# Optimization experiments

Measured on AMD Instinct MI355X. Metric: run time of the kernel, lower is better.

The kernel has to match this reference:

```python
import jax, jax.numpy as jnp
import numpy as np

K_CORR = 2048        # num_correspondences (init kwarg)
MAX_CORR = 8192      # static pad size for the variable-length nonzero output
THRES_START = 0.5
THRES_STEP = 0.01


def setup_inputs() -> dict:
    key = jax.random.key(0)
    k1, k2, k3 = jax.random.split(key, 3)
    N = M = 8193  # 8192 superpoints + 1 dustbin
    # shift so exp(scores) is mostly well below the 0.5 starting threshold,
    # making the iterative threshold search actually iterate (as in practice
    # with log-domain OT scores)
    matching_scores = jax.random.normal(k1, (N, M), dtype=jnp.float32) - 5.0
    ref_n2p_scores_c = jax.random.uniform(k2, (N - 1,), dtype=jnp.float32)
    src_n2p_scores_c = jax.random.uniform(k3, (M - 1,), dtype=jnp.float32)
    return {
        "matching_scores": matching_scores,
        "ref_n2p_scores_c": ref_n2p_scores_c,
        "src_n2p_scores_c": src_n2p_scores_c,
    }


def _find_thres(inner, k):
    """Replicates: while count(score[:-1,:-1] > thres) < k: thres -= 0.01."""
    def cond(t):
        return jnp.sum(inner > t) < k
    def body(t):
        return t - jnp.float32(THRES_STEP)
    return jax.lax.while_loop(cond, body, jnp.float32(THRES_START))


def reference(matching_scores, ref_n2p_scores_c, src_n2p_scores_c):
    s = jnp.exp(matching_scores)
    # n2p reweighting of the non-dustbin block, as in the torch in-place update
    inner = s[:-1, :-1] * (ref_n2p_scores_c[:, None] * src_n2p_scores_c[None, :])
    # threshold search is discrete -> not differentiated
    thres = _find_thres(jax.lax.stop_gradient(inner), K_CORR)
    mask = inner > thres
    count = jnp.sum(mask)
    # torch returns variable-length nonzero in row-major order; we pad to MAX_CORR
    r, c = jnp.nonzero(mask, size=MAX_CORR, fill_value=0)
    valid = jnp.arange(MAX_CORR) < count
    corr_scores = jnp.where(valid, inner[r, c], 0.0)
    ref_corr_indices = jnp.where(valid, r, -1)
    src_corr_indices = jnp.where(valid, c, -1)
    return ref_corr_indices, src_corr_indices, corr_scores
```

## Files before the change

### kernel.cpp

```cpp
#include <hip/hip_runtime.h>

#define NROWS 8192
#define NCOLS 8192
#define LDIM  8193
#define NBINS 64
#define KCORR 2048
#define MAXC  8192
#define CAP   192
#define FCUT_LOG (-2.5257286443082556f)

#define NQUAD   16781312
#define TILEQ   1024
#define NTILES  16388
#define NGROUPS 262208

__device__ __forceinline__ float inner_val(float m, float rr, float sc) {
    float p = rr * sc;
    return expf(m) * p;
}

__device__ __forceinline__ void fold_thresholds(float* t) {
    float tv = 0.5f;
    for (int n = 0; n < NBINS; ++n) { t[n] = tv; tv = tv - 0.01f; }
}

__device__ __forceinline__ int exact_bin(float v, const float* t) {
    int g = (int)floorf((0.5f - v) * 100.0f) + 1;
    g = (g < 0) ? 0 : ((g > NBINS) ? NBINS : g);
    while (g < NBINS && t[g] >= v) ++g;
    while (g > 0 && t[g - 1] < v) --g;
    return (g > 63) ? 63 : g;
}

__global__ void init_kernel(float* __restrict__ out, unsigned* __restrict__ hist,
                            unsigned* __restrict__ hist2,
                            unsigned* __restrict__ candcnt,
                            unsigned* __restrict__ fullmode) {
    int i = blockIdx.x * blockDim.x + threadIdx.x;
    if (i < 2 * MAXC)       out[i] = -1.0f;
    else if (i < 3 * MAXC)  out[i] = 0.0f;
    if (i < NBINS) { hist[i] = 0u; hist2[i] = 0u; }
    if (i == NBINS) *fullmode = 0u;
    if (i < NROWS) candcnt[i] = 0u;
}

__global__ __launch_bounds__(256) void scan_mask_kernel(
    const float* __restrict__ ms, unsigned long long* __restrict__ masks)
{
    const int tid = threadIdx.x;
    const int lane = tid & 63, wv = tid >> 6;
    const float4* m4 = (const float4*)ms;
    const int g = gridDim.x;

    float4 b0[4], b1[4];
    auto issue = [&](int t, float4* B) {
        const float4* p = m4 + (size_t)t * TILEQ + tid;
        #pragma unroll
        for (int k = 0; k < 4; ++k) B[k] = p[k * 256];
    };
    auto emit = [&](int t, const float4* B) {
        unsigned long long mk0 = __ballot((B[0].x > FCUT_LOG) | (B[0].y > FCUT_LOG) |
                                          (B[0].z > FCUT_LOG) | (B[0].w > FCUT_LOG));
        unsigned long long mk1 = __ballot((B[1].x > FCUT_LOG) | (B[1].y > FCUT_LOG) |
                                          (B[1].z > FCUT_LOG) | (B[1].w > FCUT_LOG));
        unsigned long long mk2 = __ballot((B[2].x > FCUT_LOG) | (B[2].y > FCUT_LOG) |
                                          (B[2].z > FCUT_LOG) | (B[2].w > FCUT_LOG));
        unsigned long long mk3 = __ballot((B[3].x > FCUT_LOG) | (B[3].y > FCUT_LOG) |
                                          (B[3].z > FCUT_LOG) | (B[3].w > FCUT_LOG));
        unsigned long long val = (lane & 2) ? ((lane & 1) ? mk3 : mk2)
                                            : ((lane & 1) ? mk1 : mk0);
        if (lane < 4)
            masks[(size_t)t * 16 + wv * 4 + lane] = val;
    };

    int t = blockIdx.x;
    issue(t, b0);
    while (true) {
        int t1 = t + g;
        if (t1 < NTILES) issue(t1, b1);
        emit(t, b0);
        t = t1;
        if (t >= NTILES) break;
        int t2 = t + g;
        if (t2 < NTILES) issue(t2, b0);
        emit(t, b1);
        t = t2;
        if (t >= NTILES) break;
    }
}

__global__ __launch_bounds__(256) void expand_kernel(
    const float* __restrict__ ms, const float* __restrict__ refs,
    const float* __restrict__ srcs, const unsigned long long* __restrict__ masks,
    unsigned* __restrict__ hist, unsigned* __restrict__ candcnt,
    unsigned* __restrict__ cand_col, float* __restrict__ cand_v, int use_cand)
{
    __shared__ float t[NBINS];
    __shared__ unsigned sub[NBINS];
    int tid = threadIdx.x;
    if (tid == 0) fold_thresholds(t);
    if (tid < NBINS) sub[tid] = 0u;
    __syncthreads();

    for (int i = blockIdx.x * 256 + tid; i < NGROUPS; i += gridDim.x * 256) {
        unsigned long long mask = masks[i];
        if (!mask) continue;
        int tile = i >> 4, r = i & 15, w = r >> 2, k = r & 3;
        int quadBase = tile * TILEQ + k * 256 + w * 64;
        while (mask) {
            int b = __ffsll((long long)mask) - 1;
            mask &= mask - 1;
            int q = quadBase + b;
            float4 v4 = ((const float4*)ms)[q];
            int e0 = q * 4;
            #pragma unroll
            for (int j = 0; j < 4; ++j) {
                float m = (j == 0) ? v4.x : (j == 1) ? v4.y : (j == 2) ? v4.z : v4.w;
                if (!(m > FCUT_LOG)) continue;
                unsigned e = (unsigned)(e0 + j);
                unsigned row = e / 8193u;
                unsigned col = e - row * 8193u;
                if (row >= NROWS || col >= NCOLS) continue;
                float v = inner_val(m, refs[row], srcs[col]);
                atomicAdd(&sub[exact_bin(v, t)], 1u);
                if (use_cand) {
                    unsigned slot = atomicAdd(&candcnt[row], 1u);
                    if (slot < CAP) {
                        cand_col[(size_t)row * CAP + slot] = col;
                        cand_v[(size_t)row * CAP + slot]   = v;
                    }
                }
            }
        }
    }
    __syncthreads();
    if (tid < NBINS && sub[tid]) atomicAdd(&hist[tid], sub[tid]);
}

__global__ void mid_kernel(const unsigned* __restrict__ hist,
                           float* __restrict__ thres, unsigned* __restrict__ nstar,
                           unsigned* __restrict__ fullmode) {
    int tid = threadIdx.x;
    unsigned cum = hist[tid];
    #pragma unroll
    for (int off = 1; off < 64; off <<= 1) {
        unsigned u = __shfl_up(cum, off);
        if (tid >= off) cum += u;
    }
    unsigned long long mk = __ballot(cum >= (unsigned)KCORR);
    if (tid == 0) {
        int nsel = mk ? (int)(__ffsll((long long)mk) - 1) : NBINS;
        if (nsel <= 41) {
            float tv = 0.5f;
            for (int n = 0; n < nsel; ++n) tv = tv - 0.01f;
            *thres = tv; *nstar = (unsigned)nsel; *fullmode = 0u;
        } else {
            *fullmode = 1u; *nstar = 63u; *thres = -1e30f;
        }
    }
}

__global__ __launch_bounds__(256) void fb_hist_kernel(
    const float* __restrict__ ms, const float* __restrict__ refs,
    const float* __restrict__ srcs, const unsigned* __restrict__ fullmode,
    unsigned* __restrict__ hist2)
{
    if (*fullmode == 0u) return;
    __shared__ float t[NBINS];
    __shared__ unsigned sub[64 * 65];
    int tid = threadIdx.x, lane = tid & 63;
    if (tid == 0) fold_thresholds(t);
    for (int i = tid; i < 64 * 65; i += 256) sub[i] = 0u;
    __syncthreads();
    unsigned* mysub = sub + lane * 65;
    for (int q = blockIdx.x * 256 + tid; q < NQUAD; q += gridDim.x * 256) {
        float4 v4 = ((const float4*)ms)[q];
        int e0 = q * 4;
        #pragma unroll
        for (int j = 0; j < 4; ++j) {
            float m = (j == 0) ? v4.x : (j == 1) ? v4.y : (j == 2) ? v4.z : v4.w;
            unsigned e = (unsigned)(e0 + j);
            unsigned row = e / 8193u;
            unsigned col = e - row * 8193u;
            if (row >= NROWS || col >= NCOLS) continue;
            float v = inner_val(m, refs[row], srcs[col]);
            atomicAdd(&mysub[exact_bin(v, t)], 1u);
        }
    }
    __syncthreads();
    if (tid < 64) {
        unsigned s = 0;
        for (int c = 0; c < 64; ++c) s += sub[c * 65 + tid];
        if (s) atomicAdd(&hist2[tid], s);
    }
}

__global__ void mid2_kernel(const unsigned* __restrict__ hist2,
                            const unsigned* __restrict__ fullmode,
                            float* __restrict__ thres, unsigned* __restrict__ nstar) {
    if (*fullmode == 0u) return;
    int tid = threadIdx.x;
    unsigned cum = hist2[tid];
    #pragma unroll
    for (int off = 1; off < 64; off <<= 1) {
        unsigned u = __shfl_up(cum, off);
        if (tid >= off) cum += u;
    }
    unsigned long long mk = __ballot(cum >= (unsigned)KCORR);
    if (tid == 0) {
        int nsel = mk ? (int)(__ffsll((long long)mk) - 1) : (NBINS - 1);
        float tv = 0.5f;
        for (int n = 0; n < nsel; ++n) tv = tv - 0.01f;
        *thres = tv; *nstar = (unsigned)nsel;
    }
}

__global__ __launch_bounds__(256) void rowcnt_kernel(
    const float* __restrict__ ms, const float* __restrict__ refs,
    const float* __restrict__ srcs, const float* __restrict__ thresp,
    const unsigned* __restrict__ fullmode, const unsigned* __restrict__ candcnt,
    const float* __restrict__ cand_v, unsigned* __restrict__ rowcnt, int use_cand)
{
    if (!use_cand || *fullmode != 0u) return;
    int tid = threadIdx.x, wv = tid >> 6, lane = tid & 63;
    int row = blockIdx.x * 4 + wv;
    float th = *thresp;
    unsigned C = candcnt[row];
    unsigned c = 0;
    if (C <= CAP) {
        const float* cv = cand_v + (size_t)row * CAP;
        for (unsigned i = lane; i < C; i += 64) c += (cv[i] > th) ? 1u : 0u;
    } else {
        float rr = refs[row];
        const float* mrow = ms + (size_t)row * LDIM;
        for (int col = lane; col < NCOLS; col += 64)
            c += (inner_val(mrow[col], rr, srcs[col]) > th) ? 1u : 0u;
    }
    #pragma unroll
    for (int off = 32; off > 0; off >>= 1) c += __shfl_down(c, off);
    if (lane == 0) rowcnt[row] = c;
}

__global__ __launch_bounds__(256) void count2_kernel(
    const float* __restrict__ ms, const float* __restrict__ refs,
    const float* __restrict__ srcs, const float* __restrict__ thresp,
    const unsigned* __restrict__ fullmode, unsigned* __restrict__ rowcnt,
    int use_cand)
{
    if (use_cand && *fullmode == 0u) return;
    __shared__ unsigned tot;
    float th = *thresp;
    for (int r4 = 0; r4 < 4; ++r4) {
        int row = blockIdx.x * 4 + r4;
        if (threadIdx.x == 0) tot = 0;
        __syncthreads();
        float rr = refs[row];
        const float* mrow = ms + (size_t)row * LDIM;
        unsigned c = 0;
        for (int col = threadIdx.x; col < NCOLS; col += 256)
            c += (inner_val(mrow[col], rr, srcs[col]) > th) ? 1u : 0u;
        atomicAdd(&tot, c);
        __syncthreads();
        if (threadIdx.x == 0) rowcnt[row] = tot;
        __syncthreads();
    }
}

__global__ __launch_bounds__(1024) void scan_kernel(
    const unsigned* __restrict__ rowcnt, unsigned* __restrict__ rowoff)
{
    __shared__ unsigned ssum[1024];
    int tid = threadIdx.x;
    int r0 = tid * 8;
    unsigned c[8], s = 0;
    #pragma unroll
    for (int k = 0; k < 8; ++k) { c[k] = rowcnt[r0 + k]; s += c[k]; }
    ssum[tid] = s;
    __syncthreads();
    for (int off = 1; off < 1024; off <<= 1) {
        unsigned v = (tid >= off) ? ssum[tid - off] : 0u;
        __syncthreads();
        ssum[tid] += v;
        __syncthreads();
    }
    unsigned excl = ssum[tid] - s;
    #pragma unroll
    for (int k = 0; k < 8; ++k) { rowoff[r0 + k] = excl; excl += c[k]; }
    if (tid == 1023) rowoff[NROWS] = excl;
}

__global__ __launch_bounds__(256) void cwrite_kernel(
    const float* __restrict__ ms, const float* __restrict__ refs,
    const float* __restrict__ srcs, const float* __restrict__ thresp,
    const unsigned* __restrict__ fullmode, const unsigned* __restrict__ rowoff,
    const unsigned* __restrict__ candcnt, const unsigned* __restrict__ cand_col,
    const float* __restrict__ cand_v, float* __restrict__ out, int use_cand)
{
    __shared__ unsigned s_col[4][64];
    __shared__ float    s_val[4][64];
    int tid = threadIdx.x, wv = tid >> 6, lane = tid & 63;
    int row = blockIdx.x * 4 + wv;
    unsigned base = rowoff[row], next = rowoff[row + 1];
    if (base == next || base >= MAXC) return;
    float th = *thresp;
    unsigned k = next - base;
    bool full = (!use_cand) || (*fullmode != 0u) || (candcnt[row] > CAP) || (k > 64);

    if (!full) {
        unsigned C = candcnt[row];
        const unsigned* cc = cand_col + (size_t)row * CAP;
        const float*    cv = cand_v  + (size_t)row * CAP;
        unsigned nrun = 0;
        for (unsigned c0 = 0; c0 < C; c0 += 64) {
            unsigned i = c0 + lane;
            bool sel = false; unsigned col = 0; float v = 0.f;
            if (i < C) { col = cc[i]; v = cv[i]; sel = (v > th); }
            unsigned long long mk = __ballot(sel);
            if (sel) {
                unsigned idx = nrun + (unsigned)__popcll(mk & ((1ull << lane) - 1ull));
                if (idx < 64) { s_col[wv][idx] = col; s_val[wv][idx] = v; }
            }
            nrun += (unsigned)__popcll(mk);
        }
        __builtin_amdgcn_s_waitcnt(0);
        __builtin_amdgcn_wave_barrier();
        unsigned kk = (nrun < k) ? nrun : k;
        if (kk > 64) kk = 64;
        if (lane < (int)kk) {
            unsigned mycol = s_col[wv][lane];
            float    myval = s_val[wv][lane];
            unsigned rank = 0;
            for (unsigned j = 0; j < kk; ++j)
                rank += (s_col[wv][j] < mycol) ? 1u : 0u;
            unsigned pos = base + rank;
            if (pos < MAXC) {
                out[pos]            = (float)row;
                out[MAXC + pos]     = (float)mycol;
                out[2 * MAXC + pos] = myval;
            }
        }
        return;
    }

    float rr = refs[row];
    const float* mrow = ms + (size_t)row * LDIM;
    unsigned running = base;
    for (int c0 = 0; c0 < NCOLS && running < next && running < MAXC; c0 += 64) {
        int col = c0 + lane;
        float v = inner_val(mrow[col], rr, srcs[col]);
        bool pred = v > th;
        unsigned long long mk = __ballot(pred);
        if (pred) {
            unsigned pos = running + (unsigned)__popcll(mk & ((1ull << lane) - 1ull));
            if (pos < MAXC) {
                out[pos]            = (float)row;
                out[MAXC + pos]     = (float)col;
                out[2 * MAXC + pos] = v;
            }
        }
        running += (unsigned)__popcll(mk);
    }
}

extern "C" void kernel_launch(void* const* d_in, const int* in_sizes, int n_in,
                              void* d_out, int out_size, void* d_ws, size_t ws_size,
                              hipStream_t stream) {
    const float* ms  = (const float*)d_in[0];
    const float* ref = (const float*)d_in[1];
    const float* src = (const float*)d_in[2];
    float* out = (float*)d_out;

    char* w = (char*)d_ws;
    unsigned* hist     = (unsigned*)(w);
    unsigned* hist2    = (unsigned*)(w + 256);
    float*    thres    = (float*)(w + 512);
    unsigned* nstar    = (unsigned*)(w + 516);
    unsigned* fullmode = (unsigned*)(w + 520);
    unsigned* rowcnt   = (unsigned*)(w + 1024);
    unsigned* rowoff   = (unsigned*)(w + 1024 + NROWS * 4);
    size_t cc_off = (1024 + (size_t)NROWS * 4 + (size_t)(NROWS + 1) * 4 + 255) & ~(size_t)255;
    unsigned* candcnt = (unsigned*)(w + cc_off);
    size_t mk_off  = cc_off + (size_t)NROWS * 4;
    unsigned long long* masks = (unsigned long long*)(w + mk_off);
    size_t col_off = mk_off + (size_t)NGROUPS * 8;
    unsigned* cand_col = (unsigned*)(w + col_off);
    size_t cv_off  = col_off + (size_t)NROWS * CAP * 4;
    float* cand_v  = (float*)(w + cv_off);
    size_t end_off = cv_off + (size_t)NROWS * CAP * 4;

    int use_mask = (ws_size >= col_off) ? 1 : 0;
    int use_cand = (ws_size >= end_off) ? 1 : 0;

    init_kernel<<<96, 256, 0, stream>>>(out, hist, hist2, candcnt, fullmode);
    if (use_mask) {
        scan_mask_kernel<<<2048, 256, 0, stream>>>(ms, masks);
        expand_kernel<<<1024, 256, 0, stream>>>(ms, ref, src, masks, hist,
                                                candcnt, cand_col, cand_v, use_cand);
    }
    mid_kernel<<<1, 64, 0, stream>>>(hist, thres, nstar, fullmode);
    fb_hist_kernel<<<2048, 256, 0, stream>>>(ms, ref, src, fullmode, hist2);
    mid2_kernel<<<1, 64, 0, stream>>>(hist2, fullmode, thres, nstar);
    rowcnt_kernel<<<NROWS / 4, 256, 0, stream>>>(ms, ref, src, thres, fullmode,
                                                 candcnt, cand_v, rowcnt, use_cand);
    count2_kernel<<<NROWS / 4, 256, 0, stream>>>(ms, ref, src, thres, fullmode,
                                                 rowcnt, use_cand);
    scan_kernel<<<1, 1024, 0, stream>>>(rowcnt, rowoff);
    cwrite_kernel<<<NROWS / 4, 256, 0, stream>>>(ms, ref, src, thres, fullmode,
                                                 rowoff, candcnt, cand_col,
                                                 cand_v, out, use_cand);
}
```

Measured before the change: 431.0 us.

## Fuse mask scan and candidate expansion into one LDS-pipelined streaming kernel

Replaces the two-pass scan_mask + expand kernels with a single dscan kernel. Each wave streams its strided slice of the score matrix into an 8-deep LDS ring via global_load_lds with manual vmcnt waits, and collects above-cutoff elements into a per-block shared buffer. That buffer is then processed for the histogram and per-row candidates. This removes the mask buffer round trip and the second gather read of the matrix. A per-block capacity overflow flag forces the existing full fallback path, which adds a correctness dependency on the candidate density staying under the capacity.

```diff
diff --git a/kernel.cpp b/kernel.cpp
--- a/kernel.cpp
+++ b/kernel.cpp
@@ -7,12 +7,12 @@
 #define KCORR 2048
 #define MAXC  8192
 #define CAP   192
+#define BCAP  448
 #define FCUT_LOG (-2.5257286443082556f)
 
 #define NQUAD   16781312
-#define TILEQ   1024
-#define NTILES  16388
-#define NGROUPS 262208
+#define TOTW    8192
+#define QSTRIDE 524288
 
 __device__ __forceinline__ float inner_val(float m, float rr, float sc) {
     float p = rr * sc;
@@ -32,112 +32,105 @@
     return (g > 63) ? 63 : g;
 }
 
+__device__ __forceinline__ void gl2lds16(const void* g, void* l) {
+    __builtin_amdgcn_global_load_lds(
+        (const __attribute__((address_space(1))) void*)g,
+        (__attribute__((address_space(3))) void*)l, 16, 0, 0);
+}
+
 __global__ void init_kernel(float* __restrict__ out, unsigned* __restrict__ hist,
                             unsigned* __restrict__ hist2,
                             unsigned* __restrict__ candcnt,
-                            unsigned* __restrict__ fullmode) {
+                            unsigned* __restrict__ fullmode,
+                            unsigned* __restrict__ ovfl) {
     int i = blockIdx.x * blockDim.x + threadIdx.x;
     if (i < 2 * MAXC)       out[i] = -1.0f;
     else if (i < 3 * MAXC)  out[i] = 0.0f;
     if (i < NBINS) { hist[i] = 0u; hist2[i] = 0u; }
-    if (i == NBINS) *fullmode = 0u;
+    if (i == NBINS) { *fullmode = 0u; *ovfl = 0u; }
     if (i < NROWS) candcnt[i] = 0u;
 }
 
-__global__ __launch_bounds__(256) void scan_mask_kernel(
-    const float* __restrict__ ms, unsigned long long* __restrict__ masks)
-{
-    const int tid = threadIdx.x;
-    const int lane = tid & 63, wv = tid >> 6;
-    const float4* m4 = (const float4*)ms;
-    const int g = gridDim.x;
-
-    float4 b0[4], b1[4];
-    auto issue = [&](int t, float4* B) {
-        const float4* p = m4 + (size_t)t * TILEQ + tid;
-        #pragma unroll
-        for (int k = 0; k < 4; ++k) B[k] = p[k * 256];
-    };
-    auto emit = [&](int t, const float4* B) {
-        unsigned long long mk0 = __ballot((B[0].x > FCUT_LOG) | (B[0].y > FCUT_LOG) |
-                                          (B[0].z > FCUT_LOG) | (B[0].w > FCUT_LOG));
-        unsigned long long mk1 = __ballot((B[1].x > FCUT_LOG) | (B[1].y > FCUT_LOG) |
-                                          (B[1].z > FCUT_LOG) | (B[1].w > FCUT_LOG));
-        unsigned long long mk2 = __ballot((B[2].x > FCUT_LOG) | (B[2].y > FCUT_LOG) |
-                                          (B[2].z > FCUT_LOG) | (B[2].w > FCUT_LOG));
-        unsigned long long mk3 = __ballot((B[3].x > FCUT_LOG) | (B[3].y > FCUT_LOG) |
-                                          (B[3].z > FCUT_LOG) | (B[3].w > FCUT_LOG));
-        unsigned long long val = (lane & 2) ? ((lane & 1) ? mk3 : mk2)
-                                            : ((lane & 1) ? mk1 : mk0);
-        if (lane < 4)
-            masks[(size_t)t * 16 + wv * 4 + lane] = val;
-    };
-
-    int t = blockIdx.x;
-    issue(t, b0);
-    while (true) {
-        int t1 = t + g;
-        if (t1 < NTILES) issue(t1, b1);
-        emit(t, b0);
-        t = t1;
-        if (t >= NTILES) break;
-        int t2 = t + g;
-        if (t2 < NTILES) issue(t2, b0);
-        emit(t, b1);
-        t = t2;
-        if (t >= NTILES) break;
-    }
-}
-
-__global__ __launch_bounds__(256) void expand_kernel(
-    const float* __restrict__ ms, const float* __restrict__ refs,
-    const float* __restrict__ srcs, const unsigned long long* __restrict__ masks,
-    unsigned* __restrict__ hist, unsigned* __restrict__ candcnt,
-    unsigned* __restrict__ cand_col, float* __restrict__ cand_v, int use_cand)
-{
+__global__ __launch_bounds__(256) void dscan_kernel(
+    const float* __restrict__ ms, const float* __restrict__ refs,
+    const float* __restrict__ srcs, unsigned* __restrict__ hist,
+    unsigned* __restrict__ candcnt, unsigned* __restrict__ cand_col,
+    float* __restrict__ cand_v, unsigned* __restrict__ ovfl, int use_cand)
+{
+    __shared__ float ring[4 * 8 * 256];
     __shared__ float t[NBINS];
     __shared__ unsigned sub[NBINS];
-    int tid = threadIdx.x;
-    if (tid == 0) fold_thresholds(t);
+    __shared__ unsigned s_cnt;
+    __shared__ uint2 pairs[BCAP];
+
+    int tid = threadIdx.x, wv = tid >> 6, lane = tid & 63;
+    if (tid == 0) { fold_thresholds(t); s_cnt = 0u; }
     if (tid < NBINS) sub[tid] = 0u;
     __syncthreads();
 
-    for (int i = blockIdx.x * 256 + tid; i < NGROUPS; i += gridDim.x * 256) {
-        unsigned long long mask = masks[i];
-        if (!mask) continue;
-        int tile = i >> 4, r = i & 15, w = r >> 2, k = r & 3;
-        int quadBase = tile * TILEQ + k * 256 + w * 64;
-        while (mask) {
-            int b = __ffsll((long long)mask) - 1;
-            mask &= mask - 1;
-            int q = quadBase + b;
-            float4 v4 = ((const float4*)ms)[q];
-            int e0 = q * 4;
-            #pragma unroll
-            for (int j = 0; j < 4; ++j) {
-                float m = (j == 0) ? v4.x : (j == 1) ? v4.y : (j == 2) ? v4.z : v4.w;
-                if (!(m > FCUT_LOG)) continue;
-                unsigned e = (unsigned)(e0 + j);
-                unsigned row = e / 8193u;
-                unsigned col = e - row * 8193u;
-                if (row >= NROWS || col >= NCOLS) continue;
-                float v = inner_val(m, refs[row], srcs[col]);
-                atomicAdd(&sub[exact_bin(v, t)], 1u);
-                if (use_cand) {
-                    unsigned slot = atomicAdd(&candcnt[row], 1u);
-                    if (slot < CAP) {
-                        cand_col[(size_t)row * CAP + slot] = col;
-                        cand_v[(size_t)row * CAP + slot]   = v;
-                    }
+    int W = blockIdx.x * 4 + wv;
+    const float4* m4 = (const float4*)ms;
+    float* myring = &ring[wv * (8 * 256)];
+    int nsteps = 32 + ((W < 64) ? 1 : 0);
+
+    auto pushp = [&](unsigned e, float m) {
+        unsigned slot = atomicAdd(&s_cnt, 1u);
+        if (slot < BCAP) pairs[slot] = make_uint2(e, __float_as_uint(m));
+    };
+    auto issue = [&](int s) {
+        gl2lds16(m4 + (size_t)s * QSTRIDE + (size_t)W * 64 + lane,
+                 &myring[(s & 7) * 256]);
+    };
+
+    #pragma unroll
+    for (int s = 0; s < 7; ++s) issue(s);
+    for (int s = 0; s < nsteps; ++s) {
+        if (s + 7 < nsteps) {
+            issue(s + 7);
+            asm volatile("s_waitcnt vmcnt(7)" ::: "memory");
+        } else {
+            asm volatile("s_waitcnt vmcnt(0)" ::: "memory");
+        }
+        float4 q = *(const float4*)&myring[(s & 7) * 256 + lane * 4];
+        bool a0 = q.x > FCUT_LOG, a1 = q.y > FCUT_LOG;
+        bool a2 = q.z > FCUT_LOG, a3 = q.w > FCUT_LOG;
+        if (a0 | a1 | a2 | a3) {
+            unsigned e0 = ((unsigned)s * QSTRIDE + (unsigned)W * 64 + (unsigned)lane) * 4u;
+            if (a0) pushp(e0 + 0, q.x);
+            if (a1) pushp(e0 + 1, q.y);
+            if (a2) pushp(e0 + 2, q.z);
+            if (a3) pushp(e0 + 3, q.w);
+        }
+    }
+    __syncthreads();
+
+    unsigned C = s_cnt;
+    unsigned Cc = (C < BCAP) ? C : BCAP;
+    for (unsigned i = tid; i < Cc; i += 256) {
+        uint2 pr = pairs[i];
+        unsigned e = pr.x;
+        float m = __uint_as_float(pr.y);
+        unsigned row = e / 8193u;
+        unsigned col = e - row * 8193u;
+        if (row < NROWS && col < NCOLS) {
+            float v = inner_val(m, refs[row], srcs[col]);
+            atomicAdd(&sub[exact_bin(v, t)], 1u);
+            if (use_cand) {
+                unsigned slot = atomicAdd(&candcnt[row], 1u);
+                if (slot < CAP) {
+                    cand_col[(size_t)row * CAP + slot] = col;
+                    cand_v[(size_t)row * CAP + slot]   = v;
                 }
             }
         }
     }
+    if (tid == 0 && C > BCAP) atomicOr(ovfl, 1u);
     __syncthreads();
     if (tid < NBINS && sub[tid]) atomicAdd(&hist[tid], sub[tid]);
 }
 
 __global__ void mid_kernel(const unsigned* __restrict__ hist,
+                           const unsigned* __restrict__ ovfl,
                            float* __restrict__ thres, unsigned* __restrict__ nstar,
                            unsigned* __restrict__ fullmode) {
     int tid = threadIdx.x;
@@ -150,7 +143,7 @@
     unsigned long long mk = __ballot(cum >= (unsigned)KCORR);
     if (tid == 0) {
         int nsel = mk ? (int)(__ffsll((long long)mk) - 1) : NBINS;
-        if (nsel <= 41) {
+        if (nsel <= 41 && *ovfl == 0u) {
             float tv = 0.5f;
             for (int n = 0; n < nsel; ++n) tv = tv - 0.01f;
             *thres = tv; *nstar = (unsigned)nsel; *fullmode = 0u;
@@ -376,28 +369,23 @@
     float*    thres    = (float*)(w + 512);
     unsigned* nstar    = (unsigned*)(w + 516);
     unsigned* fullmode = (unsigned*)(w + 520);
+    unsigned* ovfl     = (unsigned*)(w + 524);
     unsigned* rowcnt   = (unsigned*)(w + 1024);
     unsigned* rowoff   = (unsigned*)(w + 1024 + NROWS * 4);
     size_t cc_off = (1024 + (size_t)NROWS * 4 + (size_t)(NROWS + 1) * 4 + 255) & ~(size_t)255;
     unsigned* candcnt = (unsigned*)(w + cc_off);
-    size_t mk_off  = cc_off + (size_t)NROWS * 4;
-    unsigned long long* masks = (unsigned long long*)(w + mk_off);
-    size_t col_off = mk_off + (size_t)NGROUPS * 8;
+    size_t col_off = cc_off + (size_t)NROWS * 4;
     unsigned* cand_col = (unsigned*)(w + col_off);
     size_t cv_off  = col_off + (size_t)NROWS * CAP * 4;
     float* cand_v  = (float*)(w + cv_off);
     size_t end_off = cv_off + (size_t)NROWS * CAP * 4;
 
-    int use_mask = (ws_size >= col_off) ? 1 : 0;
     int use_cand = (ws_size >= end_off) ? 1 : 0;
 
-    init_kernel<<<96, 256, 0, stream>>>(out, hist, hist2, candcnt, fullmode);
-    if (use_mask) {
-        scan_mask_kernel<<<2048, 256, 0, stream>>>(ms, masks);
-        expand_kernel<<<1024, 256, 0, stream>>>(ms, ref, src, masks, hist,
-                                                candcnt, cand_col, cand_v, use_cand);
-    }
-    mid_kernel<<<1, 64, 0, stream>>>(hist, thres, nstar, fullmode);
+    init_kernel<<<96, 256, 0, stream>>>(out, hist, hist2, candcnt, fullmode, ovfl);
+    dscan_kernel<<<2048, 256, 0, stream>>>(ms, ref, src, hist, candcnt,
+                                           cand_col, cand_v, ovfl, use_cand);
+    mid_kernel<<<1, 64, 0, stream>>>(hist, ovfl, thres, nstar, fullmode);
     fb_hist_kernel<<<2048, 256, 0, stream>>>(ms, ref, src, fullmode, hist2);
     mid2_kernel<<<1, 64, 0, stream>>>(hist2, fullmode, thres, nstar);
     rowcnt_kernel<<<NROWS / 4, 256, 0, stream>>>(ms, ref, src, thres, fullmode,
```

Result: no change. 426.6 us (-1.0%).
